# Optimization experiments

Measured on AMD Instinct MI355X. Metric: run time of the kernel, lower is better.

Reference implementation:

```python
import jax, jax.numpy as jnp
import numpy as np

H = 512   # hidden_state_sizes
E = 512   # embedding_size
L = 2     # num_rnn_layers
VGG = 4096


def gru_cell(x, h, Wu, bu, Wr, br, Wc, bc):
    # stacked = cat(x, h) along features; rows of W: first input, then hidden
    s = jnp.concatenate([x, h], axis=1)
    r = jax.nn.sigmoid(s @ Wr + br)
    u = jax.nn.sigmoid(s @ Wu + bu)
    s1 = jnp.concatenate([x, r * h], axis=1)
    c = jnp.tanh(s1 @ Wc + bc)
    return u * h + (1.0 - u) * c


def setup_inputs() -> dict:
    key = jax.random.key(0)
    ks = jax.random.split(key, 10)
    B, T, V = 128, 40, 10000
    N = E + H  # concat width (layer0: E+H == H+H since E==H)
    sc = float(np.sqrt(1.0 / N))
    return dict(
        xTokens=jax.random.randint(ks[0], (B, T), 0, V),
        vgg_fc7=jax.random.normal(ks[1], (B, VGG), jnp.float32),
        embedding=jax.random.normal(ks[2], (V, E), jnp.float32) * 0.02,
        W_in=jax.random.normal(ks[3], (VGG, H), jnp.float32) * float(np.sqrt(1.0 / VGG)),
        b_in=jnp.zeros((H,), jnp.float32),
        W_u=jax.random.normal(ks[4], (L, N, H), jnp.float32) * sc,
        b_u=jnp.zeros((L, H), jnp.float32),
        W_r=jax.random.normal(ks[5], (L, N, H), jnp.float32) * sc,
        b_r=jnp.zeros((L, H), jnp.float32),
        W_c=jax.random.normal(ks[6], (L, N, H), jnp.float32) * sc,
        b_c=jnp.zeros((L, H), jnp.float32),
        W_out=jax.random.normal(ks[7], (H, V), jnp.float32) * float(np.sqrt(1.0 / H)),
        b_out=jnp.zeros((V,), jnp.float32),
    )


def reference(xTokens, vgg_fc7, embedding, W_in, b_in, W_u, b_u, W_r, b_r,
              W_c, b_c, W_out, b_out):
    # initial hidden state from image features, shared across rnn layers
    h0 = jnp.tanh(vgg_fc7 @ W_in + b_in)                # [B,H]
    h = jnp.broadcast_to(h0, (L,) + h0.shape)           # [L,B,H]
    x = embedding[xTokens]                              # [B,T,E]
    xs = jnp.swapaxes(x, 0, 1)                          # [T,B,E] (scan over time)

    def step(h, xt):
        hs = []
        inp = xt
        for j in range(L):  # small fixed layer loop
            hj = gru_cell(inp, h[j], W_u[j], b_u[j], W_r[j], b_r[j], W_c[j], b_c[j])
            hs.append(hj)
            inp = hj
        logit = inp @ W_out + b_out                     # [B,V]
        return jnp.stack(hs), logit

    h_final, logits = jax.lax.scan(step, h, xs)         # logits [T,B,V]
    return jnp.swapaxes(logits, 0, 1), h_final
```

## Files before the change

kernel.cpp:

```cpp
#include <hip/hip_runtime.h>
#include <hip/hip_bf16.h>
#include <math.h>

typedef __bf16 bf16_t;
typedef __bf16 bf16x8 __attribute__((ext_vector_type(8)));
typedef float  f32x4 __attribute__((ext_vector_type(4)));
typedef float  f4    __attribute__((ext_vector_type(4)));
typedef float  f2    __attribute__((ext_vector_type(2)));
typedef unsigned short u16x4 __attribute__((ext_vector_type(4)));
typedef unsigned long long u64;

#define HS  512
#define BB  128
#define TT  40
#define VV  10000
#define VGGN 4096
#define SLOT ((size_t)65536)
#define NBLK 96
#define NGRID 256

#define CL(h, idx) ((((h) * 164) + (idx)) * 64)
#define CRH0(h,s) CL(h, (s))
#define CHB0(h,s) CL(h, 41 + (s))
#define CRH1(h,s) CL(h, 82 + (s))
#define CHB1(h,s) CL(h, 123 + (s))
#define NSYNCW (328 * 64)

__device__ __forceinline__ void cst64(void* p, u64 v) {
  __hip_atomic_store((u64*)p, v, __ATOMIC_RELAXED, __HIP_MEMORY_SCOPE_AGENT);
}

__device__ __forceinline__ void slot_inc(unsigned* sync, int line)
{
  __syncthreads();
  asm volatile("" ::: "memory");
  if (threadIdx.x == 0)
    __hip_atomic_fetch_add(&sync[line], 1u, __ATOMIC_RELAXED,
                           __HIP_MEMORY_SCOPE_AGENT);
}

template<int SLP>
__device__ __forceinline__ void slot_wait(unsigned* sync, int line,
                                          unsigned target)
{
  if (threadIdx.x == 0) {
    while (__hip_atomic_load(&sync[line], __ATOMIC_RELAXED,
                             __HIP_MEMORY_SCOPE_AGENT) < target)
      __builtin_amdgcn_s_sleep(SLP);
  }
  asm volatile("" ::: "memory");
  __syncthreads();
}

template<int SLP>
__device__ __forceinline__ void slot_wait2(unsigned* sync, int lineA,
                                           unsigned tA, int lineB, unsigned tB)
{
  if (threadIdx.x == 0) {
    while (__hip_atomic_load(&sync[lineA], __ATOMIC_RELAXED,
                             __HIP_MEMORY_SCOPE_AGENT) < tA)
      __builtin_amdgcn_s_sleep(SLP);
    while (__hip_atomic_load(&sync[lineB], __ATOMIC_RELAXED,
                             __HIP_MEMORY_SCOPE_AGENT) < tB)
      __builtin_amdgcn_s_sleep(SLP);
  }
  asm volatile("" ::: "memory");
  __syncthreads();
}

__global__ void zero_sync(unsigned* p)
{
  for (int i = threadIdx.x; i < NSYNCW; i += 256) p[i] = 0u;
}

__global__ __launch_bounds__(256) void gemm_bt(
    const bf16_t* __restrict__ A, const bf16_t* __restrict__ Bt,
    const float* __restrict__ bias, float* __restrict__ C,
    int Nvalid, int ldc, int permute_tb)
{
  const int bm = blockIdx.x * 128, bn = blockIdx.y * 128;
  const int tid = threadIdx.x;
  const int wave = tid >> 6, lane = tid & 63;
  const int wm = (wave >> 1) * 64, wn = (wave & 1) * 64;
  const int l15 = lane & 15, kg = lane >> 4;
  const bf16_t* Ap = A + (size_t)(bm + wm + l15) * 512 + kg * 8;
  const bf16_t* Bp = Bt + (size_t)(bn + wn + l15) * 512 + kg * 8;
  f32x4 acc[4][4];
#pragma unroll
  for (int i = 0; i < 4; ++i)
#pragma unroll
    for (int j = 0; j < 4; ++j)
#pragma unroll
      for (int e = 0; e < 4; ++e) acc[i][j][e] = 0.f;

  for (int kk = 0; kk < 512; kk += 32) {
    bf16x8 a[4], b[4];
#pragma unroll
    for (int i = 0; i < 4; ++i) a[i] = *(const bf16x8*)(Ap + (size_t)i * 16 * 512 + kk);
#pragma unroll
    for (int j = 0; j < 4; ++j) b[j] = *(const bf16x8*)(Bp + (size_t)j * 16 * 512 + kk);
#pragma unroll
    for (int i = 0; i < 4; ++i)
#pragma unroll
      for (int j = 0; j < 4; ++j)
        acc[i][j] = __builtin_amdgcn_mfma_f32_16x16x32_bf16(a[i], b[j], acc[i][j], 0, 0, 0);
  }

#pragma unroll
  for (int fm = 0; fm < 4; ++fm) {
#pragma unroll
    for (int fn = 0; fn < 4; ++fn) {
      int n = bn + wn + fn * 16 + l15;
      if (n >= Nvalid) continue;
      float bv = bias ? bias[n] : 0.f;
#pragma unroll
      for (int e = 0; e < 4; ++e) {
        int m = bm + wm + fm * 16 + kg * 4 + e;
        int orow = permute_tb ? ((m & 127) * TT + (m >> 7)) : m;
        C[(size_t)orow * ldc + n] = acc[fm][fn][e] + bv;
      }
    }
  }
}

struct PArgs {
  const bf16_t *Btru0, *Bt1ru, *Btc0, *Btc1;
  const float  *xg0, *bu, *br, *bc, *hs0init;
  bf16_t *hb0_seq, *hb1_seq, *rh0s, *rh1s;
  const bf16_t *Wto;
  const float  *bo;
  float *out, *out_hfin;
  unsigned *sync;
};

template<int K, int NF>
__device__ __forceinline__ void tile_gemm64(
    const bf16_t* __restrict__ A0, const bf16_t* __restrict__ A1,
    const bf16_t* Bs, int wave, int lane, f32x4 (&acc)[NF])
{
  const int l15 = lane & 15, kg = lane >> 4;
  const int mw = wave * 16;
#pragma unroll
  for (int f = 0; f < NF; ++f)
#pragma unroll
    for (int e = 0; e < 4; ++e) acc[f][e] = 0.f;

#pragma unroll
  for (int kk = 0; kk < K; kk += 32) {
    const bf16_t* Asrc = (kk < 512) ? A0 : A1;
    const int kc = (kk < 512 ? kk : kk - 512) + kg * 8;
    bf16x8 a = *(const bf16x8*)(Asrc + (size_t)(mw + l15) * 512 + kc);
    bf16x8 b[NF];
#pragma unroll
    for (int f = 0; f < NF; ++f) {
      int row = f * 16 + l15;
      int byteoff = row * (2 * K) + ((2 * kk + 16 * kg) ^ ((row & 7) << 4));
      b[f] = *(const bf16x8*)((const char*)Bs + byteoff);
    }
#pragma unroll
    for (int f = 0; f < NF; ++f)
      acc[f] = __builtin_amdgcn_mfma_f32_16x16x32_bf16(a, b[f], acc[f], 0, 0, 0);
  }
}

template<int C>
__device__ __forceinline__ void publish64(
    bf16_t* dst, int row0, int n0, float (&v)[2][4],
    unsigned short (*tb)[36], int wave, int lane, int tid)
{
  const int l15 = lane & 15, kg = lane >> 4;
  const int mw = wave * 16;
  constexpr int NFp = C / 16;
#pragma unroll
  for (int f = 0; f < NFp; ++f)
#pragma unroll
    for (int e = 0; e < 4; ++e)
      tb[mw + kg * 4 + e][f * 16 + l15] =
          __builtin_bit_cast(unsigned short, (bf16_t)v[f][e]);
  __syncthreads();
  constexpr int NU = 64 * C / 4;
  constexpr int IT = (NU + 255) / 256;
#pragma unroll
  for (int it = 0; it < IT; ++it) {
    int lin = it * 256 + tid;
    if (lin < NU) {
      int row = lin / (C / 4);
      int cc  = (lin % (C / 4)) * 4;
      u16x4 pk = { tb[row][cc], tb[row][cc + 1], tb[row][cc + 2], tb[row][cc + 3] };
      cst64(dst + (size_t)(row0 + row) * 512 + n0 + cc, __builtin_bit_cast(u64, pk));
    }
  }
}

__global__ __launch_bounds__(256) void gru_persist(PArgs P)
{
  const int bid = blockIdx.x, tid = threadIdx.x;
  const int wave = tid >> 6, lane = tid & 63;
  const int l15 = lane & 15, kg = lane >> 4;
  unsigned* sync = P.sync;

  __threadfence();
  __syncthreads();

  if (bid >= NBLK) {
    const int w = bid - NBLK;
    const int wm = (wave >> 1) * 64, wn = (wave & 1) * 64;
    for (int tau = w; tau < TT * 79; tau += (NGRID - NBLK)) {
      const int t = tau / 79, nb = tau % 79;
      slot_wait2<64>(sync, CHB1(0, t + 1), 32u, CHB1(1, t + 1), 32u);
      const bf16_t* A = P.hb1_seq + (size_t)(t + 1) * SLOT;
      const bf16_t* Bp = P.Wto + (size_t)(nb * 128 + wn + l15) * 512 + kg * 8;
      f32x4 acc[4][4];
#pragma unroll
      for (int i = 0; i < 4; ++i)
#pragma unroll
        for (int j = 0; j < 4; ++j)
#pragma unroll
          for (int e = 0; e < 4; ++e) acc[i][j][e] = 0.f;
      for (int kk = 0; kk < 512; kk += 32) {
        bf16x8 a[4], b[4];
#pragma unroll
        for (int i = 0; i < 4; ++i)
          a[i] = *(const bf16x8*)(A + (size_t)(wm + i * 16 + l15) * 512 + kk + kg * 8);
#pragma unroll
        for (int j = 0; j < 4; ++j)
          b[j] = *(const bf16x8*)(Bp + (size_t)j * 16 * 512 + kk);
#pragma unroll
        for (int i = 0; i < 4; ++i)
#pragma unroll
          for (int j = 0; j < 4; ++j)
            acc[i][j] = __builtin_amdgcn_mfma_f32_16x16x32_bf16(a[i], b[j], acc[i][j], 0, 0, 0);
      }
#pragma unroll
      for (int fm = 0; fm < 4; ++fm) {
#pragma unroll
        for (int fn = 0; fn < 4; ++fn) {
          int n = nb * 128 + wn + fn * 16 + l15;
          if (n >= VV) continue;
          float bv = P.bo[n];
#pragma unroll
          for (int e = 0; e < 4; ++e) {
            int b_row = wm + fm * 16 + kg * 4 + e;
            P.out[(size_t)(b_row * TT + t) * VV + n] = acc[fm][fn][e] + bv;
          }
        }
      }
      __syncthreads();
    }
    return;
  }

  const int half = bid / 48;
  const int b2   = bid % 48;
  const int row0 = half * 64;
  const bool L0 = (b2 < 16);
  const int q  = L0 ? b2 : b2 - 16;
  const int n0 = L0 ? q * 32 : q * 16;
  const int mw = wave * 16;

  __shared__ bf16_t Bs[49152];
  __shared__ unsigned short tb[64][36];
  bf16_t* BsRU = Bs;
  bf16_t* BsC  = Bs + 32768;

  if (L0) {
    for (int c = tid; c < 4096; c += 256) {
      int row = c >> 6, cb = (c & 63) * 16;
      const bf16_t* src = (row < 32) ? P.Btru0 + (size_t)(n0 + row) * 512
                                     : P.Btru0 + (size_t)(512 + n0 + row - 32) * 512;
      *(f4*)((char*)BsRU + row * 1024 + (cb ^ ((row & 7) << 4))) =
          *(const f4*)((const char*)src + cb);
    }
    for (int c = tid; c < 2048; c += 256) {
      int row = c >> 6, cb = (c & 63) * 16;
      const bf16_t* src = P.Btc0 + (size_t)(n0 + row) * 512;
      *(f4*)((char*)BsC + row * 1024 + (cb ^ ((row & 7) << 4))) =
          *(const f4*)((const char*)src + cb);
    }
  } else {
    for (int c = tid; c < 4096; c += 256) {
      int row = c >> 7, cb = (c & 127) * 16;
      const bf16_t* src = (row < 16) ? P.Bt1ru + (size_t)(n0 + row) * 1024
                                     : P.Bt1ru + (size_t)(512 + n0 + row - 16) * 1024;
      *(f4*)((char*)BsRU + row * 2048 + (cb ^ ((row & 7) << 4))) =
          *(const f4*)((const char*)src + cb);
    }
    for (int c = tid; c < 2048; c += 256) {
      int row = c >> 7, cb = (c & 127) * 16;
      const bf16_t* src = P.Btc1 + (size_t)(n0 + row) * 1024;
      *(f4*)((char*)BsC + row * 2048 + (cb ^ ((row & 7) << 4))) =
          *(const f4*)((const char*)src + cb);
    }
  }
  __syncthreads();

  const int NFh = L0 ? 2 : 1;
  float hreg[2][4], ureg[2][4], rhv[2][4];
#pragma unroll
  for (int f = 0; f < 2; ++f)
#pragma unroll
    for (int e = 0; e < 4; ++e) {
      int row = row0 + mw + kg * 4 + e;
      hreg[f][e] = (f < NFh)
          ? P.hs0init[(size_t)row * 512 + n0 + f * 16 + l15] : 0.f;
      ureg[f][e] = 0.f; rhv[f][e] = 0.f;
    }

  if (L0) {
    for (int s = 0; s < 40; ++s) {
      const float* xg = P.xg0 + (size_t)s * 128 * 1536;
      float xvu[2][4], xvr[2][4];
#pragma unroll
      for (int f = 0; f < 2; ++f)
#pragma unroll
        for (int e = 0; e < 4; ++e) {
          int row = row0 + mw + kg * 4 + e;
          int col = n0 + f * 16 + l15;
          xvu[f][e] = xg[(size_t)row * 1536 + col];
          xvr[f][e] = xg[(size_t)row * 1536 + 512 + col];
        }
      if (s >= 1) slot_wait<8>(sync, CHB0(half, s), 16u);
      f32x4 acc4[4];
      const bf16_t* A0 = P.hb0_seq + (size_t)s * SLOT + (size_t)row0 * 512;
      tile_gemm64<512, 4>(A0, A0, BsRU, wave, lane, acc4);
#pragma unroll
      for (int f = 0; f < 2; ++f)
#pragma unroll
        for (int e = 0; e < 4; ++e) {
          float pu = acc4[f][e]     + xvu[f][e];
          float pr = acc4[f + 2][e] + xvr[f][e];
          ureg[f][e] = 1.f / (1.f + expf(-pu));
          rhv[f][e]  = (1.f / (1.f + expf(-pr))) * hreg[f][e];
        }
      publish64<32>(P.rh0s + (size_t)s * SLOT, row0, n0, rhv, tb, wave, lane, tid);
      slot_inc(sync, CRH0(half, s));
      float xvc[2][4];
#pragma unroll
      for (int f = 0; f < 2; ++f)
#pragma unroll
        for (int e = 0; e < 4; ++e) {
          int row = row0 + mw + kg * 4 + e;
          int col = n0 + f * 16 + l15;
          xvc[f][e] = xg[(size_t)row * 1536 + 1024 + col];
        }
      slot_wait<8>(sync, CRH0(half, s), 16u);

      f32x4 acc2[2];
      const bf16_t* Arh = P.rh0s + (size_t)s * SLOT + (size_t)row0 * 512;
      tile_gemm64<512, 2>(Arh, Arh, BsC, wave, lane, acc2);
#pragma unroll
      for (int f = 0; f < 2; ++f)
#pragma unroll
        for (int e = 0; e < 4; ++e) {
          float c = tanhf(acc2[f][e] + xvc[f][e]);
          float u = ureg[f][e];
          hreg[f][e] = u * hreg[f][e] + (1.f - u) * c;
          rhv[f][e] = hreg[f][e];
        }
      publish64<32>(P.hb0_seq + (size_t)(s + 1) * SLOT, row0, n0, rhv, tb, wave, lane, tid);
      slot_inc(sync, CHB0(half, s + 1));
    }
  } else {
    const float bvu = P.bu[512 + n0 + l15];
    const float bvr = P.br[512 + n0 + l15];
    const float bvc = P.bc[512 + n0 + l15];
    for (int s = 1; s <= 40; ++s) {
      if (s >= 2) slot_wait2<8>(sync, CHB0(half, s), 16u, CHB1(half, s - 1), 32u);
      else        slot_wait<8>(sync, CHB0(half, 1), 16u);
      f32x4 acc2[2];
      tile_gemm64<1024, 2>(P.hb0_seq + (size_t)s * SLOT + (size_t)row0 * 512,
                           P.hb1_seq + (size_t)(s - 1) * SLOT + (size_t)row0 * 512,
                           BsRU, wave, lane, acc2);
#pragma unroll
      for (int e = 0; e < 4; ++e) {
        float pu = acc2[0][e] + bvu;
        float pr = acc2[1][e] + bvr;
        ureg[0][e] = 1.f / (1.f + expf(-pu));
        rhv[0][e]  = (1.f / (1.f + expf(-pr))) * hreg[0][e];
      }
      publish64<16>(P.rh1s + (size_t)s * SLOT, row0, n0, rhv, tb, wave, lane, tid);
      slot_inc(sync, CRH1(half, s));
      slot_wait<8>(sync, CRH1(half, s), 32u);

      f32x4 acc1[1];
      tile_gemm64<1024, 1>(P.hb0_seq + (size_t)s * SLOT + (size_t)row0 * 512,
                           P.rh1s + (size_t)s * SLOT + (size_t)row0 * 512,
                           BsC, wave, lane, acc1);
#pragma unroll
      for (int e = 0; e < 4; ++e) {
        float c = tanhf(acc1[0][e] + bvc);
        float u = ureg[0][e];
        hreg[0][e] = u * hreg[0][e] + (1.f - u) * c;
        rhv[0][e] = hreg[0][e];
      }
      publish64<16>(P.hb1_seq + (size_t)s * SLOT, row0, n0, rhv, tb, wave, lane, tid);
      slot_inc(sync, CHB1(half, s));
    }
  }

  float* dst = P.out_hfin + (L0 ? 0 : 65536);
#pragma unroll
  for (int f = 0; f < 2; ++f)
    if (f < NFh)
#pragma unroll
      for (int e = 0; e < 4; ++e) {
        int row = row0 + mw + kg * 4 + e;
        dst[(size_t)row * 512 + n0 + f * 16 + l15] = hreg[f][e];
      }
}

__global__ __launch_bounds__(256) void h0_gemm(
    const bf16_t* __restrict__ vggb, const bf16_t* __restrict__ Wint,
    float* __restrict__ part)
{
  const int bn = blockIdx.x * 128, z = blockIdx.y, k0 = z * 512;
  const int tid = threadIdx.x;
  const int wave = tid >> 6, lane = tid & 63;
  const int wm = (wave >> 1) * 64, wn = (wave & 1) * 64;
  const int l15 = lane & 15, kg = lane >> 4;
  const bf16_t* Ap = vggb + (size_t)(wm + l15) * 4096 + k0 + kg * 8;
  const bf16_t* Bp = Wint + (size_t)(bn + wn + l15) * 4096 + k0 + kg * 8;
  f32x4 acc[4][4];
#pragma unroll
  for (int i = 0; i < 4; ++i)
#pragma unroll
    for (int j = 0; j < 4; ++j)
#pragma unroll
      for (int e = 0; e < 4; ++e) acc[i][j][e] = 0.f;
  for (int kk = 0; kk < 512; kk += 32) {
    bf16x8 a[4], b[4];
#pragma unroll
    for (int i = 0; i < 4; ++i) a[i] = *(const bf16x8*)(Ap + (size_t)i * 16 * 4096 + kk);
#pragma unroll
    for (int j = 0; j < 4; ++j) b[j] = *(const bf16x8*)(Bp + (size_t)j * 16 * 4096 + kk);
#pragma unroll
    for (int i = 0; i < 4; ++i)
#pragma unroll
      for (int j = 0; j < 4; ++j)
        acc[i][j] = __builtin_amdgcn_mfma_f32_16x16x32_bf16(a[i], b[j], acc[i][j], 0, 0, 0);
  }
#pragma unroll
  for (int fm = 0; fm < 4; ++fm)
#pragma unroll
    for (int fn = 0; fn < 4; ++fn) {
      int n = bn + wn + fn * 16 + l15;
#pragma unroll
      for (int e = 0; e < 4; ++e) {
        int m = wm + fm * 16 + kg * 4 + e;
        part[(size_t)z * SLOT + m * 512 + n] = acc[fm][fn][e];
      }
    }
}

__global__ void h0_fin(const float* __restrict__ part, const float* __restrict__ bin,
                       float* __restrict__ hs0init,
                       bf16_t* __restrict__ hb00, bf16_t* __restrict__ hb10)
{
  int i = blockIdx.x * 256 + threadIdx.x;
  int n = i & 511;
  float s = bin[n];
#pragma unroll
  for (int z = 0; z < 8; ++z) s += part[(size_t)z * SLOT + i];
  float v = tanhf(s);
  hs0init[i] = v;
  hb00[i] = (bf16_t)v; hb10[i] = (bf16_t)v;
}

__global__ void conv_bf16(const float* __restrict__ src, bf16_t* __restrict__ dst)
{
  int i = blockIdx.x * 256 + threadIdx.x;
  f4 v = ((const f4*)src)[i];
  dst[i * 4 + 0] = (bf16_t)v[0]; dst[i * 4 + 1] = (bf16_t)v[1];
  dst[i * 4 + 2] = (bf16_t)v[2]; dst[i * 4 + 3] = (bf16_t)v[3];
}

__global__ void gather_emb(const int* __restrict__ tok, const float* __restrict__ emb,
                           bf16_t* __restrict__ A)
{
  int m = blockIdx.x;
  int t = m >> 7, b = m & 127;
  int tk = tok[b * TT + t];
  const float* src = emb + (size_t)tk * 512;
  int i = threadIdx.x;
  f4 v = *(const f4*)(src + i * 4);
  bf16_t* dst = A + (size_t)m * 512 + i * 4;
  dst[0] = (bf16_t)v[0]; dst[1] = (bf16_t)v[1];
  dst[2] = (bf16_t)v[2]; dst[3] = (bf16_t)v[3];
}

struct TJob { const float* src; bf16_t* dst; int K; int dstld; };
struct TJobs10 { TJob j[10]; };
__global__ void transpose_gen(TJobs10 jobs)
{
  TJob jb = jobs.j[blockIdx.z];
  int k0 = blockIdx.x * 32;
  if (k0 >= jb.K) return;
  int n0 = blockIdx.y * 32;
  __shared__ float tile[32][33];
  int tx = threadIdx.x, ty = threadIdx.y;
#pragma unroll
  for (int r = 0; r < 4; ++r)
    tile[ty + 8 * r][tx] = jb.src[(size_t)(k0 + ty + 8 * r) * 512 + n0 + tx];
  __syncthreads();
#pragma unroll
  for (int r = 0; r < 4; ++r)
    jb.dst[(size_t)(n0 + ty + 8 * r) * jb.dstld + k0 + tx] = (bf16_t)tile[tx][ty + 8 * r];
}

__global__ void transpose_wout(const float* __restrict__ W, bf16_t* __restrict__ dst)
{
  __shared__ float tile[32][33];
  int k0 = blockIdx.x * 32, n0 = blockIdx.y * 32;
  int tx = threadIdx.x, ty = threadIdx.y;
#pragma unroll
  for (int r = 0; r < 4; ++r) {
    int n = n0 + tx;
    tile[ty + 8 * r][tx] = (n < VV) ? W[(size_t)(k0 + ty + 8 * r) * VV + n] : 0.f;
  }
  __syncthreads();
#pragma unroll
  for (int r = 0; r < 4; ++r)
    dst[(size_t)(n0 + ty + 8 * r) * 512 + k0 + tx] = (bf16_t)tile[tx][ty + 8 * r];
}

__global__ void build_xbias(const float* __restrict__ bu, const float* __restrict__ br,
                            const float* __restrict__ bc, float* __restrict__ xb)
{
  int i = blockIdx.x * 256 + threadIdx.x;
  if (i < 2 * 1536) {
    int j = i / 1536, qq = i % 1536;
    int g = qq >> 9, n = qq & 511;
    const float* src = (g == 0) ? bu : (g == 1) ? br : bc;
    xb[i] = src[j * 512 + n];
  }
}

extern "C" void kernel_launch(void* const* d_in, const int* in_sizes, int n_in,
                              void* d_out, int out_size, void* d_ws, size_t ws_size,
                              hipStream_t stream)
{
  const int*   tok = (const int*)  d_in[0];
  const float* vgg = (const float*)d_in[1];
  const float* emb = (const float*)d_in[2];
  const float* Win = (const float*)d_in[3];
  const float* bin = (const float*)d_in[4];
  const float* Wu  = (const float*)d_in[5];
  const float* bu  = (const float*)d_in[6];
  const float* Wr  = (const float*)d_in[7];
  const float* br  = (const float*)d_in[8];
  const float* Wc  = (const float*)d_in[9];
  const float* bc  = (const float*)d_in[10];
  const float* Wo  = (const float*)d_in[11];
  const float* bo  = (const float*)d_in[12];
  float* out = (float*)d_out;

  size_t off = 0;
  auto alloc = [&](size_t bytes) -> void* {
    void* p = (char*)d_ws + off;
    off += (bytes + 255) & ~(size_t)255;
    return p;
  };
  float*  hs0init = (float*) alloc(SLOT * 4);
  bf16_t* rh0s  = (bf16_t*)alloc(41 * SLOT * 2);
  bf16_t* rh1s  = (bf16_t*)alloc(41 * SLOT * 2);
  bf16_t* hb0_seq = (bf16_t*)alloc(41 * SLOT * 2);
  bf16_t* hb1_seq = (bf16_t*)alloc(41 * SLOT * 2);
  bf16_t* Aemb  = (bf16_t*)alloc((size_t)TT * BB * 512 * 2);
  float*  xg0   = (float*) alloc((size_t)TT * BB * 1536 * 4);
  bf16_t* Btx0  = (bf16_t*)alloc((size_t)1536 * 512 * 2);
  bf16_t* Btru0 = (bf16_t*)alloc((size_t)1024 * 512 * 2);
  bf16_t* Btc0  = (bf16_t*)alloc((size_t)512 * 512 * 2);
  bf16_t* Bt1ru = (bf16_t*)alloc((size_t)1024 * 1024 * 2);
  bf16_t* Btc1  = (bf16_t*)alloc((size_t)512 * 1024 * 2);
  bf16_t* Wto   = (bf16_t*)alloc((size_t)10112 * 512 * 2);
  bf16_t* Wint  = (bf16_t*)alloc((size_t)512 * 4096 * 2);
  bf16_t* vggb  = (bf16_t*)alloc((size_t)128 * 4096 * 2);
  float*  h0part= (float*) alloc(8 * SLOT * 4);
  float*  xbias = (float*) alloc(2 * 1536 * 4);
  unsigned* syncws = (unsigned*) alloc(NSYNCW * 4);
  if (off > ws_size) return;

  TJobs10 tj;
  tj.j[0] = { Wu,                Btx0,                512, 512 };
  tj.j[1] = { Wr,                Btx0 + 262144,       512, 512 };
  tj.j[2] = { Wc,                Btx0 + 524288,       512, 512 };
  tj.j[3] = { Wu + 262144,       Btru0,               512, 512 };
  tj.j[4] = { Wr + 262144,       Btru0 + 262144,      512, 512 };
  tj.j[5] = { Wc + 262144,       Btc0,                512, 512 };
  tj.j[6] = { Wu + 524288,       Bt1ru,               1024, 1024 };
  tj.j[7] = { Wr + 524288,       Bt1ru + 524288,      1024, 1024 };
  tj.j[8] = { Wc + 524288,       Btc1,                1024, 1024 };
  tj.j[9] = { Win,               Wint,                4096, 4096 };
  transpose_gen<<<dim3(128, 16, 10), dim3(32, 8), 0, stream>>>(tj);
  transpose_wout<<<dim3(16, 316), dim3(32, 8), 0, stream>>>(Wo, Wto);
  build_xbias<<<12, 256, 0, stream>>>(bu, br, bc, xbias);
  gather_emb<<<TT * BB, 128, 0, stream>>>(tok, emb, Aemb);
  conv_bf16<<<512, 256, 0, stream>>>(vgg, vggb);
  zero_sync<<<1, 256, 0, stream>>>(syncws);

  h0_gemm<<<dim3(4, 8), 256, 0, stream>>>(vggb, Wint, h0part);
  h0_fin<<<256, 256, 0, stream>>>(h0part, bin, hs0init, hb0_seq, hb1_seq);

  gemm_bt<<<dim3(40, 12), 256, 0, stream>>>(Aemb, Btx0, xbias, xg0, 1536, 1536, 0);

  PArgs pa;
  pa.Btru0 = Btru0; pa.Bt1ru = Bt1ru; pa.Btc0 = Btc0; pa.Btc1 = Btc1;
  pa.xg0 = xg0; pa.bu = bu; pa.br = br; pa.bc = bc; pa.hs0init = hs0init;
  pa.hb0_seq = hb0_seq; pa.hb1_seq = hb1_seq;
  pa.rh0s = rh0s; pa.rh1s = rh1s;
  pa.Wto = Wto; pa.bo = bo; pa.out = out;
  pa.out_hfin = out + (size_t)BB * TT * VV;
  pa.sync = syncws;
  gru_persist<<<NGRID, 256, 0, stream>>>(pa);
}
```

Baseline: 619.8 us.

## Fuse input-projection GEMM into persistent kernel and merge small prep launches

Moves the layer-0 input-projection GEMM into the idle output-projection blocks of the persistent GRU kernel. Each 128-row time slice signals a per-timestep counter that the recurrent blocks wait on, so the recurrence can start before all projections finish. Several tiny prep kernels (sync zeroing, bias build, bf16 conversion, embedding gather) are merged into one launch, and the transpose work is split into two kernels with tighter grids. This removes launch overhead and serialization, at the cost of extra flag polling and atomic stores for the projection output.

```diff
diff --git a/kernel.cpp b/kernel.cpp
--- a/kernel.cpp
+++ b/kernel.cpp
@@ -24,10 +24,14 @@
 #define CHB0(h,s) CL(h, 41 + (s))
 #define CRH1(h,s) CL(h, 82 + (s))
 #define CHB1(h,s) CL(h, 123 + (s))
-#define NSYNCW (328 * 64)
+#define XGR(t)    ((328 + (t)) * 64)
+#define NSYNCW (368 * 64)
 
 __device__ __forceinline__ void cst64(void* p, u64 v) {
   __hip_atomic_store((u64*)p, v, __ATOMIC_RELAXED, __HIP_MEMORY_SCOPE_AGENT);
+}
+__device__ __forceinline__ void cst32(float* p, float v) {
+  __hip_atomic_store(p, v, __ATOMIC_RELAXED, __HIP_MEMORY_SCOPE_AGENT);
 }
 
 __device__ __forceinline__ void slot_inc(unsigned* sync, int line)
@@ -68,64 +72,50 @@
   __syncthreads();
 }
 
-__global__ void zero_sync(unsigned* p)
-{
-  for (int i = threadIdx.x; i < NSYNCW; i += 256) p[i] = 0u;
-}
-
-__global__ __launch_bounds__(256) void gemm_bt(
-    const bf16_t* __restrict__ A, const bf16_t* __restrict__ Bt,
-    const float* __restrict__ bias, float* __restrict__ C,
-    int Nvalid, int ldc, int permute_tb)
-{
-  const int bm = blockIdx.x * 128, bn = blockIdx.y * 128;
-  const int tid = threadIdx.x;
-  const int wave = tid >> 6, lane = tid & 63;
-  const int wm = (wave >> 1) * 64, wn = (wave & 1) * 64;
-  const int l15 = lane & 15, kg = lane >> 4;
-  const bf16_t* Ap = A + (size_t)(bm + wm + l15) * 512 + kg * 8;
-  const bf16_t* Bp = Bt + (size_t)(bn + wn + l15) * 512 + kg * 8;
-  f32x4 acc[4][4];
-#pragma unroll
-  for (int i = 0; i < 4; ++i)
-#pragma unroll
-    for (int j = 0; j < 4; ++j)
-#pragma unroll
-      for (int e = 0; e < 4; ++e) acc[i][j][e] = 0.f;
-
-  for (int kk = 0; kk < 512; kk += 32) {
-    bf16x8 a[4], b[4];
-#pragma unroll
-    for (int i = 0; i < 4; ++i) a[i] = *(const bf16x8*)(Ap + (size_t)i * 16 * 512 + kk);
-#pragma unroll
-    for (int j = 0; j < 4; ++j) b[j] = *(const bf16x8*)(Bp + (size_t)j * 16 * 512 + kk);
-#pragma unroll
-    for (int i = 0; i < 4; ++i)
-#pragma unroll
-      for (int j = 0; j < 4; ++j)
-        acc[i][j] = __builtin_amdgcn_mfma_f32_16x16x32_bf16(a[i], b[j], acc[i][j], 0, 0, 0);
-  }
-
-#pragma unroll
-  for (int fm = 0; fm < 4; ++fm) {
-#pragma unroll
-    for (int fn = 0; fn < 4; ++fn) {
-      int n = bn + wn + fn * 16 + l15;
-      if (n >= Nvalid) continue;
-      float bv = bias ? bias[n] : 0.f;
-#pragma unroll
-      for (int e = 0; e < 4; ++e) {
-        int m = bm + wm + fm * 16 + kg * 4 + e;
-        int orow = permute_tb ? ((m & 127) * TT + (m >> 7)) : m;
-        C[(size_t)orow * ldc + n] = acc[fm][fn][e] + bv;
-      }
-    }
+struct MiscArgs {
+  unsigned* sync;
+  const float *bu, *br, *bc;
+  float* xbias;
+  const float* vgg; bf16_t* vggb;
+  const int* tok; const float* emb; bf16_t* Aemb;
+};
+__global__ __launch_bounds__(256) void prep_misc(MiscArgs M)
+{
+  const int b = blockIdx.x, tid = threadIdx.x;
+  if (b == 0) {
+    for (int i = tid; i < NSYNCW; i += 256) M.sync[i] = 0u;
+  } else if (b < 13) {
+    int i = (b - 1) * 256 + tid;
+    if (i < 2 * 1536) {
+      int j = i / 1536, qq = i % 1536;
+      int g = qq >> 9, n = qq & 511;
+      const float* src = (g == 0) ? M.bu : (g == 1) ? M.br : M.bc;
+      M.xbias[i] = src[j * 512 + n];
+    }
+  } else if (b < 525) {
+    int i = (b - 13) * 256 + tid;
+    f4 v = ((const f4*)M.vgg)[i];
+    M.vggb[i * 4 + 0] = (bf16_t)v[0]; M.vggb[i * 4 + 1] = (bf16_t)v[1];
+    M.vggb[i * 4 + 2] = (bf16_t)v[2]; M.vggb[i * 4 + 3] = (bf16_t)v[3];
+  } else {
+    int blk = b - 525;
+    int m = blk * 2 + (tid >> 7);
+    int t = m >> 7, bb = m & 127;
+    int tk = M.tok[bb * TT + t];
+    int i = tid & 127;
+    f4 v = *(const f4*)(M.emb + (size_t)tk * 512 + i * 4);
+    bf16_t* dst = M.Aemb + (size_t)m * 512 + i * 4;
+    dst[0] = (bf16_t)v[0]; dst[1] = (bf16_t)v[1];
+    dst[2] = (bf16_t)v[2]; dst[3] = (bf16_t)v[3];
   }
 }
 
 struct PArgs {
   const bf16_t *Btru0, *Bt1ru, *Btc0, *Btc1;
-  const float  *xg0, *bu, *br, *bc, *hs0init;
+  const float  *bu, *br, *bc, *hs0init;
+  float *xg0;
+  const bf16_t *Aemb, *Btx0;
+  const float  *xbias;
   bf16_t *hb0_seq, *hb1_seq, *rh0s, *rh1s;
   const bf16_t *Wto;
   const float  *bo;
@@ -205,6 +195,47 @@
   if (bid >= NBLK) {
     const int w = bid - NBLK;
     const int wm = (wave >> 1) * 64, wn = (wave & 1) * 64;
+
+    for (int tau = w; tau < TT * 12; tau += (NGRID - NBLK)) {
+      const int t = tau / 12, nb = tau % 12;
+      const int bm = t * 128, bn = nb * 128;
+      const bf16_t* Ap = P.Aemb + (size_t)(bm + wm + l15) * 512 + kg * 8;
+      const bf16_t* Bp = P.Btx0 + (size_t)(bn + wn + l15) * 512 + kg * 8;
+      f32x4 acc[4][4];
+#pragma unroll
+      for (int i = 0; i < 4; ++i)
+#pragma unroll
+        for (int j = 0; j < 4; ++j)
+#pragma unroll
+          for (int e = 0; e < 4; ++e) acc[i][j][e] = 0.f;
+      for (int kk = 0; kk < 512; kk += 32) {
+        bf16x8 a[4], b[4];
+#pragma unroll
+        for (int i = 0; i < 4; ++i) a[i] = *(const bf16x8*)(Ap + (size_t)i * 16 * 512 + kk);
+#pragma unroll
+        for (int j = 0; j < 4; ++j) b[j] = *(const bf16x8*)(Bp + (size_t)j * 16 * 512 + kk);
+#pragma unroll
+        for (int i = 0; i < 4; ++i)
+#pragma unroll
+          for (int j = 0; j < 4; ++j)
+            acc[i][j] = __builtin_amdgcn_mfma_f32_16x16x32_bf16(a[i], b[j], acc[i][j], 0, 0, 0);
+      }
+#pragma unroll
+      for (int fm = 0; fm < 4; ++fm) {
+#pragma unroll
+        for (int fn = 0; fn < 4; ++fn) {
+          int n = bn + wn + fn * 16 + l15;
+          float bv = P.xbias[n];
+#pragma unroll
+          for (int e = 0; e < 4; ++e) {
+            int m = bm + wm + fm * 16 + kg * 4 + e;
+            cst32(&P.xg0[(size_t)m * 1536 + n], acc[fm][fn][e] + bv);
+          }
+        }
+      }
+      slot_inc(sync, XGR(t));
+    }
+
     for (int tau = w; tau < TT * 79; tau += (NGRID - NBLK)) {
       const int t = tau / 79, nb = tau % 79;
       slot_wait2<64>(sync, CHB1(0, t + 1), 32u, CHB1(1, t + 1), 32u);
@@ -308,6 +339,7 @@
 
   if (L0) {
     for (int s = 0; s < 40; ++s) {
+      slot_wait<8>(sync, XGR(s), 12u);
       const float* xg = P.xg0 + (size_t)s * 128 * 1536;
       float xvu[2][4], xvr[2][4];
 #pragma unroll
@@ -466,31 +498,9 @@
   hb00[i] = (bf16_t)v; hb10[i] = (bf16_t)v;
 }
 
-__global__ void conv_bf16(const float* __restrict__ src, bf16_t* __restrict__ dst)
-{
-  int i = blockIdx.x * 256 + threadIdx.x;
-  f4 v = ((const f4*)src)[i];
-  dst[i * 4 + 0] = (bf16_t)v[0]; dst[i * 4 + 1] = (bf16_t)v[1];
-  dst[i * 4 + 2] = (bf16_t)v[2]; dst[i * 4 + 3] = (bf16_t)v[3];
-}
-
-__global__ void gather_emb(const int* __restrict__ tok, const float* __restrict__ emb,
-                           bf16_t* __restrict__ A)
-{
-  int m = blockIdx.x;
-  int t = m >> 7, b = m & 127;
-  int tk = tok[b * TT + t];
-  const float* src = emb + (size_t)tk * 512;
-  int i = threadIdx.x;
-  f4 v = *(const f4*)(src + i * 4);
-  bf16_t* dst = A + (size_t)m * 512 + i * 4;
-  dst[0] = (bf16_t)v[0]; dst[1] = (bf16_t)v[1];
-  dst[2] = (bf16_t)v[2]; dst[3] = (bf16_t)v[3];
-}
-
 struct TJob { const float* src; bf16_t* dst; int K; int dstld; };
-struct TJobs10 { TJob j[10]; };
-__global__ void transpose_gen(TJobs10 jobs)
+struct TJobs4 { TJob j[4]; };
+__global__ void transpose_gen(TJobs4 jobs)
 {
   TJob jb = jobs.j[blockIdx.z];
   int k0 = blockIdx.x * 32;
@@ -507,6 +517,24 @@
     jb.dst[(size_t)(n0 + ty + 8 * r) * jb.dstld + k0 + tx] = (bf16_t)tile[tx][ty + 8 * r];
 }
 
+struct TJobs6 { TJob j[6]; };
+__global__ void transpose_gen6(TJobs6 jobs)
+{
+  TJob jb = jobs.j[blockIdx.z];
+  int k0 = blockIdx.x * 32;
+  if (k0 >= jb.K) return;
+  int n0 = blockIdx.y * 32;
+  __shared__ float tile[32][33];
+  int tx = threadIdx.x, ty = threadIdx.y;
+#pragma unroll
+  for (int r = 0; r < 4; ++r)
+    tile[ty + 8 * r][tx] = jb.src[(size_t)(k0 + ty + 8 * r) * 512 + n0 + tx];
+  __syncthreads();
+#pragma unroll
+  for (int r = 0; r < 4; ++r)
+    jb.dst[(size_t)(n0 + ty + 8 * r) * jb.dstld + k0 + tx] = (bf16_t)tile[tx][ty + 8 * r];
+}
+
 __global__ void transpose_wout(const float* __restrict__ W, bf16_t* __restrict__ dst)
 {
   __shared__ float tile[32][33];
@@ -521,18 +549,6 @@
 #pragma unroll
   for (int r = 0; r < 4; ++r)
     dst[(size_t)(n0 + ty + 8 * r) * 512 + k0 + tx] = (bf16_t)tile[tx][ty + 8 * r];
-}
-
-__global__ void build_xbias(const float* __restrict__ bu, const float* __restrict__ br,
-                            const float* __restrict__ bc, float* __restrict__ xb)
-{
-  int i = blockIdx.x * 256 + threadIdx.x;
-  if (i < 2 * 1536) {
-    int j = i / 1536, qq = i % 1536;
-    int g = qq >> 9, n = qq & 511;
-    const float* src = (g == 0) ? bu : (g == 1) ? br : bc;
-    xb[i] = src[j * 512 + n];
-  }
 }
 
 extern "C" void kernel_launch(void* const* d_in, const int* in_sizes, int n_in,
@@ -580,32 +596,34 @@
   unsigned* syncws = (unsigned*) alloc(NSYNCW * 4);
   if (off > ws_size) return;
 
-  TJobs10 tj;
-  tj.j[0] = { Wu,                Btx0,                512, 512 };
-  tj.j[1] = { Wr,                Btx0 + 262144,       512, 512 };
-  tj.j[2] = { Wc,                Btx0 + 524288,       512, 512 };
-  tj.j[3] = { Wu + 262144,       Btru0,               512, 512 };
-  tj.j[4] = { Wr + 262144,       Btru0 + 262144,      512, 512 };
-  tj.j[5] = { Wc + 262144,       Btc0,                512, 512 };
-  tj.j[6] = { Wu + 524288,       Bt1ru,               1024, 1024 };
-  tj.j[7] = { Wr + 524288,       Bt1ru + 524288,      1024, 1024 };
-  tj.j[8] = { Wc + 524288,       Btc1,                1024, 1024 };
-  tj.j[9] = { Win,               Wint,                4096, 4096 };
-  transpose_gen<<<dim3(128, 16, 10), dim3(32, 8), 0, stream>>>(tj);
+  MiscArgs ma;
+  ma.sync = syncws; ma.bu = bu; ma.br = br; ma.bc = bc; ma.xbias = xbias;
+  ma.vgg = vgg; ma.vggb = vggb; ma.tok = tok; ma.emb = emb; ma.Aemb = Aemb;
+  prep_misc<<<3085, 256, 0, stream>>>(ma);
+
+  TJobs4 t4;
+  t4.j[0] = { Wu,          Btx0,           512, 512 };
+  t4.j[1] = { Wr,          Btx0 + 262144,  512, 512 };
+  t4.j[2] = { Wc,          Btx0 + 524288,  512, 512 };
+  t4.j[3] = { Win,         Wint,           4096, 4096 };
+  transpose_gen<<<dim3(128, 16, 4), dim3(32, 8), 0, stream>>>(t4);
+  TJobs6 t6;
+  t6.j[0] = { Wu + 262144, Btru0,            512, 512 };
+  t6.j[1] = { Wr + 262144, Btru0 + 262144,   512, 512 };
+  t6.j[2] = { Wc + 262144, Btc0,             512, 512 };
+  t6.j[3] = { Wu + 524288, Bt1ru,            1024, 1024 };
+  t6.j[4] = { Wr + 524288, Bt1ru + 524288,   1024, 1024 };
+  t6.j[5] = { Wc + 524288, Btc1,             1024, 1024 };
+  transpose_gen6<<<dim3(32, 16, 6), dim3(32, 8), 0, stream>>>(t6);
   transpose_wout<<<dim3(16, 316), dim3(32, 8), 0, stream>>>(Wo, Wto);
-  build_xbias<<<12, 256, 0, stream>>>(bu, br, bc, xbias);
-  gather_emb<<<TT * BB, 128, 0, stream>>>(tok, emb, Aemb);
-  conv_bf16<<<512, 256, 0, stream>>>(vgg, vggb);
-  zero_sync<<<1, 256, 0, stream>>>(syncws);
 
   h0_gemm<<<dim3(4, 8), 256, 0, stream>>>(vggb, Wint, h0part);
   h0_fin<<<256, 256, 0, stream>>>(h0part, bin, hs0init, hb0_seq, hb1_seq);
 
-  gemm_bt<<<dim3(40, 12), 256, 0, stream>>>(Aemb, Btx0, xbias, xg0, 1536, 1536, 0);
-
   PArgs pa;
   pa.Btru0 = Btru0; pa.Bt1ru = Bt1ru; pa.Btc0 = Btc0; pa.Btc1 = Btc1;
-  pa.xg0 = xg0; pa.bu = bu; pa.br = br; pa.bc = bc; pa.hs0init = hs0init;
+  pa.bu = bu; pa.br = br; pa.bc = bc; pa.hs0init = hs0init;
+  pa.xg0 = xg0; pa.Aemb = Aemb; pa.Btx0 = Btx0; pa.xbias = xbias;
   pa.hb0_seq = hb0_seq; pa.hb1_seq = hb1_seq;
   pa.rh0s = rh0s; pa.rh1s = rh1s;
   pa.Wto = Wto; pa.bo = bo; pa.out = out;
```

Measured after the change: 579.0 us. -6.6%, faster.
